# Performance work log

Measured on AMD Instinct MI355X. Metric: run time of the kernel, lower is better.

Reference implementation:

```python
import jax, jax.numpy as jnp
import numpy as np

N_NODES = 50000
N_EDGES = 800000
D_IN = 256
D_H = 128
D_OUT = 2
NUM_FC = 2


def setup_inputs() -> dict:
    key = jax.random.key(0)
    ks = jax.random.split(key, 12)
    s = 0.05
    inp = {
        "x": jax.random.normal(ks[0], (N_NODES, D_IN), dtype=jnp.float32),
        "edge_index": jax.random.randint(ks[1], (2, N_EDGES), 0, N_NODES, dtype=jnp.int64),
        "W_gcn": jax.random.normal(ks[2], (D_IN, D_H), dtype=jnp.float32) * s,
        "b_gcn": jnp.zeros((D_H,), dtype=jnp.float32),
        "fc1_W": jax.random.normal(ks[3], (D_H, D_H), dtype=jnp.float32) * s,
        "fc1_b": jnp.zeros((D_H,), dtype=jnp.float32),
        "fc2_W": jax.random.normal(ks[4], (D_H, D_H), dtype=jnp.float32) * s,
        "fc2_b": jnp.zeros((D_H,), dtype=jnp.float32),
        "out_W": jax.random.normal(ks[5], (D_H, D_OUT), dtype=jnp.float32) * s,
        "out_b": jnp.zeros((D_OUT,), dtype=jnp.float32),
    }
    return inp


def _gcn_conv(x, edge_index, W, b):
    # PyG GCNConv: add self-loops, symmetric normalization D^-1/2 (A+I) D^-1/2, then aggregate X@W.
    n = x.shape[0]
    loops = jnp.arange(n, dtype=edge_index.dtype)
    src = jnp.concatenate([edge_index[0], loops])
    dst = jnp.concatenate([edge_index[1], loops])
    h = x @ W  # [N, D_H]
    deg = jax.ops.segment_sum(jnp.ones_like(dst, dtype=h.dtype), dst, num_segments=n)
    dinv = jnp.where(deg > 0, jax.lax.rsqrt(deg), 0.0)
    norm = dinv[src] * dinv[dst]  # [E+N]
    msg = h[src] * norm[:, None]
    out = jax.ops.segment_sum(msg, dst, num_segments=n)
    return out + b


def _mlp_stack(h, fc1_W, fc1_b, fc2_W, fc2_b):
    # fc -> relu (dropout is eval-mode identity)
    h = jax.nn.relu(h @ fc1_W + fc1_b)
    h = jax.nn.relu(h @ fc2_W + fc2_b)
    return h


def reference(x, edge_index, W_gcn, b_gcn, fc1_W, fc1_b, fc2_W, fc2_b, out_W, out_b):
    h = jax.nn.relu(_gcn_conv(x, edge_index, W_gcn, b_gcn))  # [N, D_H]
    h = _mlp_stack(h, fc1_W, fc1_b, fc2_W, fc2_b)
    # edge-pair gather + average
    edge_x = (h[edge_index[0]] + h[edge_index[1]]) * 0.5  # [E, D_H]
    # note: same fc weights reused, faithful to source
    edge_x = _mlp_stack(edge_x, fc1_W, fc1_b, fc2_W, fc2_b)
    scores = edge_x @ out_W + out_b  # [E, D_OUT]
    return jax.nn.log_softmax(scores, axis=1)
```

## Files before the change

kernel.cpp:

```cpp
#include <hip/hip_runtime.h>

#define NN 50000
#define NE 800000
#define DIN 256
#define DH 128
#define BCAP 64

typedef float f32x4 __attribute__((ext_vector_type(4)));
typedef __bf16 bf16x8 __attribute__((ext_vector_type(8)));
typedef unsigned short u16;
typedef unsigned int u32;

__device__ __forceinline__ u16 f2b(float f) { return __builtin_bit_cast(u16, (__bf16)f); }
__device__ __forceinline__ float lo_f(u32 u) { return (float)__builtin_bit_cast(__bf16, (u16)(u & 0xFFFFu)); }
__device__ __forceinline__ float hi_f(u32 u) { return (float)__builtin_bit_cast(__bf16, (u16)(u >> 16)); }

__device__ __forceinline__ f32x4 mfma16(bf16x8 a, bf16x8 b, f32x4 c) {
    return __builtin_amdgcn_mfma_f32_16x16x32_bf16(a, b, c, 0, 0, 0);
}

__global__ void k_prep_fill(const float* __restrict__ w1, const float* __restrict__ w2,
                            const float* __restrict__ wg,
                            u16* __restrict__ w12f, u16* __restrict__ wgf,
                            const int* __restrict__ ei,
                            int* __restrict__ cnt, int* __restrict__ bucket) {
    int b = blockIdx.x;
    if (b < 32) {
        int t = b * 256 + threadIdx.x;
        const float* src; u16* dst; int id;
        if (t < 2048)      { src = w1; dst = w12f;          id = t; }
        else if (t < 4096) { src = w2; dst = w12f + 16384;  id = t - 2048; }
        else               { src = wg; dst = wgf;           id = t - 4096; }
        int lane = id & 63, frag = id >> 6;
        int kt = frag >> 3, nt = frag & 7;
        int k0 = kt * 32 + (lane >> 4) * 8, n = nt * 16 + (lane & 15);
        u16 v[8];
#pragma unroll
        for (int j = 0; j < 8; ++j) v[j] = f2b(src[(k0 + j) * 128 + n]);
#pragma unroll
        for (int j = 0; j < 8; ++j) dst[id * 8 + j] = v[j];
    } else {
        int e = (b - 32) * 256 + threadIdx.x;
        int d = ei[NE + e];
        int pos = atomicAdd(&cnt[d], 1);
        bucket[d * BCAP + pos] = ei[e];
    }
}

__global__ __launch_bounds__(128) void k_gemm_x(const float* __restrict__ x,
                                                const u16* __restrict__ wgf,
                                                const int* __restrict__ cnt,
                                                u16* __restrict__ h0pre) {
    int wave = threadIdx.x >> 6, lane = threadIdx.x & 63;
    int l15 = lane & 15, q = lane >> 4;
    int rowBase = blockIdx.x * 64 + wave * 32;

    bf16x8 a[2][8];
#pragma unroll
    for (int mi = 0; mi < 2; ++mi) {
        int r = rowBase + mi * 16 + l15; if (r >= NN) r = NN - 1;
        const float* rp = x + (size_t)r * DIN + q * 8;
#pragma unroll
        for (int kt = 0; kt < 8; ++kt) {
            f32x4 f0 = *(const f32x4*)(rp + kt * 32);
            f32x4 f1 = *(const f32x4*)(rp + kt * 32 + 4);
            bf16x8 aa;
#pragma unroll
            for (int j = 0; j < 4; ++j) { aa[j] = (__bf16)f0[j]; aa[j + 4] = (__bf16)f1[j]; }
            a[mi][kt] = aa;
        }
    }
    f32x4 z = {0.f, 0.f, 0.f, 0.f};
    f32x4 acc[2][8];
#pragma unroll
    for (int mi = 0; mi < 2; ++mi)
#pragma unroll
        for (int nt = 0; nt < 8; ++nt) acc[mi][nt] = z;

#pragma unroll
    for (int kt = 0; kt < 8; ++kt)
#pragma unroll
        for (int nt = 0; nt < 8; ++nt) {
            bf16x8 b = *(const bf16x8*)(wgf + ((kt * 8 + nt) * 64 + lane) * 8);
            acc[0][nt] = mfma16(a[0][kt], b, acc[0][nt]);
            acc[1][nt] = mfma16(a[1][kt], b, acc[1][nt]);
        }
#pragma unroll
    for (int mi = 0; mi < 2; ++mi)
#pragma unroll
        for (int rg = 0; rg < 4; ++rg) {
            int r = rowBase + mi * 16 + q * 4 + rg;
            if (r < NN) {
                float dv = rsqrtf((float)cnt[r] + 1.0f);
#pragma unroll
                for (int nt = 0; nt < 8; ++nt)
                    h0pre[r * DH + nt * 16 + l15] = f2b(acc[mi][nt][rg] * dv);
            }
        }
}

__global__ __launch_bounds__(256) void k_aggregate(const u16* __restrict__ h0pre,
                                                   const int* __restrict__ cnt,
                                                   const int* __restrict__ bucket,
                                                   const float* __restrict__ bg,
                                                   u16* __restrict__ hA) {
    int v = blockIdx.x * 4 + (threadIdx.x >> 6);
    int lane = threadIdx.x & 63;
    const u32* h = (const u32*)h0pre;
    u32 su = h[v * 64 + lane];
    float p0[8], p1[8];
#pragma unroll
    for (int k = 0; k < 8; ++k) { p0[k] = 0.f; p1[k] = 0.f; }
    p0[0] = lo_f(su); p1[0] = hi_f(su);
    int deg = cnt[v];
    const int* bk = bucket + v * BCAP;
    int j = 0;
    for (; j + 8 <= deg; j += 8) {
        int idx[8]; u32 u[8];
#pragma unroll
        for (int k = 0; k < 8; ++k) idx[k] = bk[j + k];
#pragma unroll
        for (int k = 0; k < 8; ++k) u[k] = h[idx[k] * 64 + lane];
#pragma unroll
        for (int k = 0; k < 8; ++k) { p0[k] += lo_f(u[k]); p1[k] += hi_f(u[k]); }
    }
    for (; j + 2 <= deg; j += 2) {
        u32 ua = h[bk[j] * 64 + lane];
        u32 ub = h[bk[j + 1] * 64 + lane];
        p0[0] += lo_f(ua); p1[0] += hi_f(ua);
        p0[1] += lo_f(ub); p1[1] += hi_f(ub);
    }
    for (; j < deg; ++j) {
        u32 u = h[bk[j] * 64 + lane];
        p0[0] += lo_f(u); p1[0] += hi_f(u);
    }
#pragma unroll
    for (int k = 4; k >= 1; k >>= 1)
#pragma unroll
        for (int m = 0; m < k; ++m) { p0[m] += p0[m + k]; p1[m] += p1[m + k]; }
    float dv = rsqrtf((float)deg + 1.0f);
    float bg0 = bg[2 * lane], bg1 = bg[2 * lane + 1];
    float a0 = fmaxf(p0[0] * dv + bg0, 0.f);
    float a1 = fmaxf(p1[0] * dv + bg1, 0.f);
    ((u32*)hA)[v * 64 + lane] = (u32)f2b(a0) | ((u32)f2b(a1) << 16);
}

__global__ __launch_bounds__(256) void k_node_mlp(const u16* __restrict__ hA,
                                                  const u16* __restrict__ wf,
                                                  const float* __restrict__ b1,
                                                  const float* __restrict__ b2,
                                                  u16* __restrict__ gh) {
    __shared__ __align__(16) u16 wlds[16384];
    __shared__ __align__(16) u16 sct[4][2176];
    {
        const uint4* s = (const uint4*)wf;
        uint4* d = (uint4*)wlds;
        for (int i = threadIdx.x; i < 2048; i += 256) d[i] = s[i];
    }
    __syncthreads();
    int wave = threadIdx.x >> 6, lane = threadIdx.x & 63;
    int l15 = lane & 15, q = lane >> 4;
    int rowBase = blockIdx.x * 128 + wave * 32;
    u16* sw = sct[wave];

    bf16x8 a[2][4];
#pragma unroll
    for (int mi = 0; mi < 2; ++mi) {
        int r = rowBase + mi * 16 + l15; if (r >= NN) r = NN - 1;
        const u16* rp = hA + r * DH + q * 8;
#pragma unroll
        for (int kt = 0; kt < 4; ++kt) a[mi][kt] = *(const bf16x8*)(rp + kt * 32);
    }
    f32x4 z = {0.f, 0.f, 0.f, 0.f};
    f32x4 acc1[2][8];
#pragma unroll
    for (int mi = 0; mi < 2; ++mi)
#pragma unroll
        for (int nt = 0; nt < 8; ++nt) acc1[mi][nt] = z;
#pragma unroll
    for (int kt = 0; kt < 4; ++kt)
#pragma unroll
        for (int nt = 0; nt < 8; ++nt) {
            bf16x8 b = *(const bf16x8*)(wlds + (kt * 8 + nt) * 512 + lane * 8);
            acc1[0][nt] = mfma16(a[0][kt], b, acc1[0][nt]);
            acc1[1][nt] = mfma16(a[1][kt], b, acc1[1][nt]);
        }
    float bb1[8], bb2[8];
#pragma unroll
    for (int nt = 0; nt < 8; ++nt) { bb1[nt] = b1[nt * 16 + l15]; bb2[nt] = b2[nt * 16 + l15]; }

    bf16x8 a2[2][4];
#pragma unroll
    for (int mi = 0; mi < 2; ++mi) {
#pragma unroll
        for (int nt = 0; nt < 8; ++nt)
#pragma unroll
            for (int rg = 0; rg < 4; ++rg) {
                float v = acc1[mi][nt][rg] + bb1[nt];
                v = v > 0.f ? v : 0.f;
                sw[(q * 4 + rg) * 136 + nt * 16 + l15] = f2b(v);
            }
#pragma unroll
        for (int kt = 0; kt < 4; ++kt)
            a2[mi][kt] = *(const bf16x8*)(sw + l15 * 136 + kt * 32 + q * 8);
    }
    __syncthreads();
    {
        const uint4* s = (const uint4*)(wf + 16384);
        uint4* d = (uint4*)wlds;
        for (int i = threadIdx.x; i < 2048; i += 256) d[i] = s[i];
    }
    __syncthreads();
    f32x4 acc2[2][8];
#pragma unroll
    for (int mi = 0; mi < 2; ++mi)
#pragma unroll
        for (int nt = 0; nt < 8; ++nt) acc2[mi][nt] = z;
#pragma unroll
    for (int kt = 0; kt < 4; ++kt)
#pragma unroll
        for (int nt = 0; nt < 8; ++nt) {
            bf16x8 b = *(const bf16x8*)(wlds + (kt * 8 + nt) * 512 + lane * 8);
            acc2[0][nt] = mfma16(a2[0][kt], b, acc2[0][nt]);
            acc2[1][nt] = mfma16(a2[1][kt], b, acc2[1][nt]);
        }
    bf16x8 a3[2][4];
#pragma unroll
    for (int mi = 0; mi < 2; ++mi) {
#pragma unroll
        for (int nt = 0; nt < 8; ++nt)
#pragma unroll
            for (int rg = 0; rg < 4; ++rg) {
                float v = acc2[mi][nt][rg] + bb2[nt];
                v = v > 0.f ? v : 0.f;
                sw[(q * 4 + rg) * 136 + nt * 16 + l15] = f2b(v);
            }
#pragma unroll
        for (int kt = 0; kt < 4; ++kt)
            a3[mi][kt] = *(const bf16x8*)(sw + l15 * 136 + kt * 32 + q * 8);
    }
    __syncthreads();
    {
        const uint4* s = (const uint4*)wf;
        uint4* d = (uint4*)wlds;
        for (int i = threadIdx.x; i < 2048; i += 256) d[i] = s[i];
    }
    __syncthreads();
    f32x4 acc3[2][8];
#pragma unroll
    for (int mi = 0; mi < 2; ++mi)
#pragma unroll
        for (int nt = 0; nt < 8; ++nt) acc3[mi][nt] = z;
#pragma unroll
    for (int kt = 0; kt < 4; ++kt)
#pragma unroll
        for (int nt = 0; nt < 8; ++nt) {
            bf16x8 b = *(const bf16x8*)(wlds + (kt * 8 + nt) * 512 + lane * 8);
            acc3[0][nt] = mfma16(a3[0][kt], b, acc3[0][nt]);
            acc3[1][nt] = mfma16(a3[1][kt], b, acc3[1][nt]);
        }
#pragma unroll
    for (int mi = 0; mi < 2; ++mi)
#pragma unroll
        for (int nt = 0; nt < 8; ++nt)
#pragma unroll
            for (int rg = 0; rg < 4; ++rg) {
                int r = rowBase + mi * 16 + q * 4 + rg;
                if (r < NN)
                    gh[r * DH + nt * 16 + l15] = f2b(0.5f * acc3[mi][nt][rg] + 0.5f * bb1[nt]);
            }
}

__global__ __launch_bounds__(256, 3) void k_edge_mlp(const u16* __restrict__ gh,
                                                     const int* __restrict__ ei,
                                                     const u16* __restrict__ wf,
                                                     const float* __restrict__ b2,
                                                     const float* __restrict__ ow,
                                                     const float* __restrict__ ob,
                                                     float2* __restrict__ outp) {
    __shared__ __align__(16) u16 wlds[16384];
    {
        const uint4* s = (const uint4*)(wf + 16384);
        uint4* d = (uint4*)wlds;
        for (int i = threadIdx.x; i < 2048; i += 256) d[i] = s[i];
    }
    int wave = threadIdx.x >> 6, lane = threadIdx.x & 63;
    int l15 = lane & 15, q = lane >> 4;
    int eBase = blockIdx.x * 256 + wave * 64;

    int se[4], de[4];
#pragma unroll
    for (int ti = 0; ti < 4; ++ti) {
        int e = eBase + ti * 16 + l15;
        se[ti] = ei[e];
        de[ti] = ei[NE + e];
    }
    bf16x8 gsA[4], gdA[4], gsB[4], gdB[4];
    {
        const u16* ps = gh + se[0] * DH + q * 8;
        const u16* pd = gh + de[0] * DH + q * 8;
#pragma unroll
        for (int kt = 0; kt < 4; ++kt) {
            gsA[kt] = *(const bf16x8*)(ps + kt * 32);
            gdA[kt] = *(const bf16x8*)(pd + kt * 32);
        }
    }
    {
        const u16* ps = gh + se[1] * DH + q * 8;
        const u16* pd = gh + de[1] * DH + q * 8;
#pragma unroll
        for (int kt = 0; kt < 4; ++kt) {
            gsB[kt] = *(const bf16x8*)(ps + kt * 32);
            gdB[kt] = *(const bf16x8*)(pd + kt * 32);
        }
    }
    float bb2[8], owp0[8], owp1[8];
#pragma unroll
    for (int nt = 0; nt < 8; ++nt) {
        int k = nt * 16 + l15;
        bb2[nt] = b2[k];
        owp0[nt] = ow[2 * k];
        owp1[nt] = ow[2 * k + 1];
    }
    float ob0 = ob[0], ob1 = ob[1];
    __syncthreads();
    f32x4 z = {0.f, 0.f, 0.f, 0.f};

#pragma unroll
    for (int ti = 0; ti < 4; ++ti) {
        bf16x8 fs[4], fd[4];
#pragma unroll
        for (int kt = 0; kt < 4; ++kt) {
            fs[kt] = (ti & 1) ? gsB[kt] : gsA[kt];
            fd[kt] = (ti & 1) ? gdB[kt] : gdA[kt];
        }
        if (ti + 2 < 4) {
            const u16* ps = gh + se[ti + 2] * DH + q * 8;
            const u16* pd = gh + de[ti + 2] * DH + q * 8;
#pragma unroll
            for (int kt = 0; kt < 4; ++kt) {
                if (ti & 1) { gsB[kt] = *(const bf16x8*)(ps + kt * 32); gdB[kt] = *(const bf16x8*)(pd + kt * 32); }
                else        { gsA[kt] = *(const bf16x8*)(ps + kt * 32); gdA[kt] = *(const bf16x8*)(pd + kt * 32); }
            }
        }
        bf16x8 a2[4];
#pragma unroll
        for (int kt = 0; kt < 4; ++kt) {
            bf16x8 r;
#pragma unroll
            for (int j = 0; j < 8; ++j) {
                float t = (float)fs[kt][j] + (float)fd[kt][j];
                r[j] = (__bf16)(t > 0.f ? t : 0.f);
            }
            a2[kt] = r;
        }
        f32x4 acc2[8];
#pragma unroll
        for (int nt = 0; nt < 8; ++nt) acc2[nt] = z;
#pragma unroll
        for (int kt = 0; kt < 4; ++kt)
#pragma unroll
            for (int nt = 0; nt < 8; ++nt) {
                bf16x8 b = *(const bf16x8*)(wlds + (kt * 8 + nt) * 512 + lane * 8);
                acc2[nt] = mfma16(a2[kt], b, acc2[nt]);
            }
#pragma unroll
        for (int rg = 0; rg < 4; ++rg) {
            float p0 = 0.f, p1 = 0.f;
#pragma unroll
            for (int nt = 0; nt < 8; ++nt) {
                float t = acc2[nt][rg] + bb2[nt];
                t = t > 0.f ? t : 0.f;
                p0 += t * owp0[nt];
                p1 += t * owp1[nt];
            }
#pragma unroll
            for (int m = 1; m < 16; m <<= 1) {
                p0 += __shfl_xor(p0, m, 64);
                p1 += __shfl_xor(p1, m, 64);
            }
            if (l15 == 0) {
                int e = eBase + ti * 16 + q * 4 + rg;
                float s0 = p0 + ob0, s1 = p1 + ob1;
                float mx = fmaxf(s0, s1);
                float lse = mx + __logf(__expf(s0 - mx) + __expf(s1 - mx));
                outp[e] = make_float2(s0 - lse, s1 - lse);
            }
        }
    }
}

extern "C" void kernel_launch(void* const* d_in, const int* in_sizes, int n_in,
                              void* d_out, int out_size, void* d_ws, size_t ws_size,
                              hipStream_t stream) {
    const float* x  = (const float*)d_in[0];
    const int* ei   = (const int*)d_in[1];
    const float* wg = (const float*)d_in[2];
    const float* bg = (const float*)d_in[3];
    const float* w1 = (const float*)d_in[4];
    const float* b1 = (const float*)d_in[5];
    const float* w2 = (const float*)d_in[6];
    const float* b2 = (const float*)d_in[7];
    const float* ow = (const float*)d_in[8];
    const float* ob = (const float*)d_in[9];
    float2* out = (float2*)d_out;

    char* ws = (char*)d_ws;
    size_t off = 0;
    auto alloc = [&](size_t bytes) { void* p = ws + off; off += (bytes + 255) & ~(size_t)255; return p; };
    u16* h0      = (u16*)alloc((size_t)NN * DH * 2);
    u16* hA      = (u16*)alloc((size_t)NN * DH * 2);
    int* bucket  = (int*)alloc((size_t)NN * BCAP * 4);
    int* cnt     = (int*)alloc((size_t)NN * 4);
    u16* w12f    = (u16*)alloc(65536);
    u16* wgf     = (u16*)alloc(65536);
    u16* gh      = h0;

    hipMemsetAsync(cnt, 0, (size_t)NN * 4, stream);
    k_prep_fill<<<32 + NE / 256, 256, 0, stream>>>(w1, w2, wg, w12f, wgf, ei, cnt, bucket);
    k_gemm_x<<<(NN + 63) / 64, 128, 0, stream>>>(x, wgf, cnt, h0);
    k_aggregate<<<NN / 4, 256, 0, stream>>>(h0, cnt, bucket, bg, hA);
    k_node_mlp<<<(NN + 127) / 128, 256, 0, stream>>>(hA, w12f, b1, b2, gh);
    k_edge_mlp<<<NE / 256, 256, 0, stream>>>(gh, ei, w12f, b2, ow, ob, out);
}
```

Measured before the change: 305.1 us.

## Process edges grouped by destination bucket in edge MLP for gather locality

The edge MLP kernel now walks edges through the destination-sorted buckets (storing source and edge id pairs) instead of original edge order. Each wave handles eight destination nodes, so destination rows are reused and hit in cache. In exchange, the bucket array doubles in size, each edge needs an index lookup, the scores are written scattered by edge id, and per-wave work varies with node degree, leaving partially filled tiles.

```diff
diff --git a/kernel.cpp b/kernel.cpp
--- a/kernel.cpp
+++ b/kernel.cpp
@@ -23,7 +23,7 @@
                             const float* __restrict__ wg,
                             u16* __restrict__ w12f, u16* __restrict__ wgf,
                             const int* __restrict__ ei,
-                            int* __restrict__ cnt, int* __restrict__ bucket) {
+                            int* __restrict__ cnt, int2* __restrict__ bucket) {
     int b = blockIdx.x;
     if (b < 32) {
         int t = b * 256 + threadIdx.x;
@@ -42,8 +42,9 @@
     } else {
         int e = (b - 32) * 256 + threadIdx.x;
         int d = ei[NE + e];
+        int s = ei[e];
         int pos = atomicAdd(&cnt[d], 1);
-        bucket[d * BCAP + pos] = ei[e];
+        bucket[d * BCAP + pos] = make_int2(s, e);
     }
 }
 
@@ -101,7 +102,7 @@
 
 __global__ __launch_bounds__(256) void k_aggregate(const u16* __restrict__ h0pre,
                                                    const int* __restrict__ cnt,
-                                                   const int* __restrict__ bucket,
+                                                   const int2* __restrict__ bucket,
                                                    const float* __restrict__ bg,
                                                    u16* __restrict__ hA) {
     int v = blockIdx.x * 4 + (threadIdx.x >> 6);
@@ -113,25 +114,25 @@
     for (int k = 0; k < 8; ++k) { p0[k] = 0.f; p1[k] = 0.f; }
     p0[0] = lo_f(su); p1[0] = hi_f(su);
     int deg = cnt[v];
-    const int* bk = bucket + v * BCAP;
+    const int2* bk = bucket + v * BCAP;
     int j = 0;
     for (; j + 8 <= deg; j += 8) {
         int idx[8]; u32 u[8];
 #pragma unroll
-        for (int k = 0; k < 8; ++k) idx[k] = bk[j + k];
+        for (int k = 0; k < 8; ++k) idx[k] = bk[j + k].x;
 #pragma unroll
         for (int k = 0; k < 8; ++k) u[k] = h[idx[k] * 64 + lane];
 #pragma unroll
         for (int k = 0; k < 8; ++k) { p0[k] += lo_f(u[k]); p1[k] += hi_f(u[k]); }
     }
     for (; j + 2 <= deg; j += 2) {
-        u32 ua = h[bk[j] * 64 + lane];
-        u32 ub = h[bk[j + 1] * 64 + lane];
+        u32 ua = h[bk[j].x * 64 + lane];
+        u32 ub = h[bk[j + 1].x * 64 + lane];
         p0[0] += lo_f(ua); p1[0] += hi_f(ua);
         p0[1] += lo_f(ub); p1[1] += hi_f(ub);
     }
     for (; j < deg; ++j) {
-        u32 u = h[bk[j] * 64 + lane];
+        u32 u = h[bk[j].x * 64 + lane];
         p0[0] += lo_f(u); p1[0] += hi_f(u);
     }
 #pragma unroll
@@ -272,7 +273,8 @@
 }
 
 __global__ __launch_bounds__(256, 3) void k_edge_mlp(const u16* __restrict__ gh,
-                                                     const int* __restrict__ ei,
+                                                     const int2* __restrict__ bucket,
+                                                     const int* __restrict__ cnt,
                                                      const u16* __restrict__ wf,
                                                      const float* __restrict__ b2,
                                                      const float* __restrict__ ow,
@@ -286,28 +288,42 @@
     }
     int wave = threadIdx.x >> 6, lane = threadIdx.x & 63;
     int l15 = lane & 15, q = lane >> 4;
-    int eBase = blockIdx.x * 256 + wave * 64;
-
-    int se[4], de[4];
-#pragma unroll
-    for (int ti = 0; ti < 4; ++ti) {
-        int e = eBase + ti * 16 + l15;
-        se[ti] = ei[e];
-        de[ti] = ei[NE + e];
-    }
+    int dstBase = blockIdx.x * 32 + wave * 8;
+
+    int c = 0;
+    if (lane < 8) { int d = dstBase + lane; c = (d < NN) ? cnt[d] : 0; }
+    int s[9]; s[0] = 0;
+#pragma unroll
+    for (int i = 0; i < 8; ++i) { int ci = __shfl(c, i, 64); s[i + 1] = s[i] + ci; }
+    int T = s[8];
+    int nT = (T + 15) >> 4;
+
+    auto fetch = [&](int t, int& src, int& dst, int& e) {
+        if (t < T) {
+            int d = 0;
+#pragma unroll
+            for (int i = 1; i < 8; ++i) d += (t >= s[i]);
+            int2 be = bucket[(dstBase + d) * BCAP + (t - s[d])];
+            src = be.x; e = be.y; dst = dstBase + d;
+        } else { src = 0; dst = 0; e = -1; }
+    };
+
+    int srcA, dstA, eA, srcB, dstB, eB;
     bf16x8 gsA[4], gdA[4], gsB[4], gdB[4];
-    {
-        const u16* ps = gh + se[0] * DH + q * 8;
-        const u16* pd = gh + de[0] * DH + q * 8;
+    fetch(l15, srcA, dstA, eA);
+    {
+        const u16* ps = gh + srcA * DH + q * 8;
+        const u16* pd = gh + dstA * DH + q * 8;
 #pragma unroll
         for (int kt = 0; kt < 4; ++kt) {
             gsA[kt] = *(const bf16x8*)(ps + kt * 32);
             gdA[kt] = *(const bf16x8*)(pd + kt * 32);
         }
     }
-    {
-        const u16* ps = gh + se[1] * DH + q * 8;
-        const u16* pd = gh + de[1] * DH + q * 8;
+    fetch(16 + l15, srcB, dstB, eB);
+    {
+        const u16* ps = gh + srcB * DH + q * 8;
+        const u16* pd = gh + dstB * DH + q * 8;
 #pragma unroll
         for (int kt = 0; kt < 4; ++kt) {
             gsB[kt] = *(const bf16x8*)(ps + kt * 32);
@@ -326,21 +342,31 @@
     __syncthreads();
     f32x4 z = {0.f, 0.f, 0.f, 0.f};
 
-#pragma unroll
-    for (int ti = 0; ti < 4; ++ti) {
+    for (int t = 0; t < nT; ++t) {
         bf16x8 fs[4], fd[4];
-#pragma unroll
-        for (int kt = 0; kt < 4; ++kt) {
-            fs[kt] = (ti & 1) ? gsB[kt] : gsA[kt];
-            fd[kt] = (ti & 1) ? gdB[kt] : gdA[kt];
-        }
-        if (ti + 2 < 4) {
-            const u16* ps = gh + se[ti + 2] * DH + q * 8;
-            const u16* pd = gh + de[ti + 2] * DH + q * 8;
-#pragma unroll
-            for (int kt = 0; kt < 4; ++kt) {
-                if (ti & 1) { gsB[kt] = *(const bf16x8*)(ps + kt * 32); gdB[kt] = *(const bf16x8*)(pd + kt * 32); }
-                else        { gsA[kt] = *(const bf16x8*)(ps + kt * 32); gdA[kt] = *(const bf16x8*)(pd + kt * 32); }
+        int eCur;
+        if (t & 1) {
+#pragma unroll
+            for (int kt = 0; kt < 4; ++kt) { fs[kt] = gsB[kt]; fd[kt] = gdB[kt]; }
+            eCur = eB;
+        } else {
+#pragma unroll
+            for (int kt = 0; kt < 4; ++kt) { fs[kt] = gsA[kt]; fd[kt] = gdA[kt]; }
+            eCur = eA;
+        }
+        if (t + 2 < nT) {
+            int srcN, dstN, eN;
+            fetch((t + 2) * 16 + l15, srcN, dstN, eN);
+            const u16* ps = gh + srcN * DH + q * 8;
+            const u16* pd = gh + dstN * DH + q * 8;
+            if (t & 1) {
+#pragma unroll
+                for (int kt = 0; kt < 4; ++kt) { gsB[kt] = *(const bf16x8*)(ps + kt * 32); gdB[kt] = *(const bf16x8*)(pd + kt * 32); }
+                eB = eN;
+            } else {
+#pragma unroll
+                for (int kt = 0; kt < 4; ++kt) { gsA[kt] = *(const bf16x8*)(ps + kt * 32); gdA[kt] = *(const bf16x8*)(pd + kt * 32); }
+                eA = eN;
             }
         }
         bf16x8 a2[4];
@@ -349,8 +375,8 @@
             bf16x8 r;
 #pragma unroll
             for (int j = 0; j < 8; ++j) {
-                float t = (float)fs[kt][j] + (float)fd[kt][j];
-                r[j] = (__bf16)(t > 0.f ? t : 0.f);
+                float tt = (float)fs[kt][j] + (float)fd[kt][j];
+                r[j] = (__bf16)(tt > 0.f ? tt : 0.f);
             }
             a2[kt] = r;
         }
@@ -369,22 +395,21 @@
             float p0 = 0.f, p1 = 0.f;
 #pragma unroll
             for (int nt = 0; nt < 8; ++nt) {
-                float t = acc2[nt][rg] + bb2[nt];
-                t = t > 0.f ? t : 0.f;
-                p0 += t * owp0[nt];
-                p1 += t * owp1[nt];
+                float tt = acc2[nt][rg] + bb2[nt];
+                tt = tt > 0.f ? tt : 0.f;
+                p0 += tt * owp0[nt];
+                p1 += tt * owp1[nt];
             }
 #pragma unroll
             for (int m = 1; m < 16; m <<= 1) {
                 p0 += __shfl_xor(p0, m, 64);
                 p1 += __shfl_xor(p1, m, 64);
             }
-            if (l15 == 0) {
-                int e = eBase + ti * 16 + q * 4 + rg;
+            if (l15 == q * 4 + rg && eCur >= 0) {
                 float s0 = p0 + ob0, s1 = p1 + ob1;
                 float mx = fmaxf(s0, s1);
                 float lse = mx + __logf(__expf(s0 - mx) + __expf(s1 - mx));
-                outp[e] = make_float2(s0 - lse, s1 - lse);
+                outp[eCur] = make_float2(s0 - lse, s1 - lse);
             }
         }
     }
@@ -410,7 +435,7 @@
     auto alloc = [&](size_t bytes) { void* p = ws + off; off += (bytes + 255) & ~(size_t)255; return p; };
     u16* h0      = (u16*)alloc((size_t)NN * DH * 2);
     u16* hA      = (u16*)alloc((size_t)NN * DH * 2);
-    int* bucket  = (int*)alloc((size_t)NN * BCAP * 4);
+    int2* bucket = (int2*)alloc((size_t)NN * BCAP * 8);
     int* cnt     = (int*)alloc((size_t)NN * 4);
     u16* w12f    = (u16*)alloc(65536);
     u16* wgf     = (u16*)alloc(65536);
@@ -421,5 +446,5 @@
     k_gemm_x<<<(NN + 63) / 64, 128, 0, stream>>>(x, wgf, cnt, h0);
     k_aggregate<<<NN / 4, 256, 0, stream>>>(h0, cnt, bucket, bg, hA);
     k_node_mlp<<<(NN + 127) / 128, 256, 0, stream>>>(hA, w12f, b1, b2, gh);
-    k_edge_mlp<<<NE / 256, 256, 0, stream>>>(gh, ei, w12f, b2, ow, ob, out);
-}
+    k_edge_mlp<<<(NN + 31) / 32, 256, 0, stream>>>(gh, bucket, cnt, w12f, b2, ow, ob, out);
+}
```

Result: slower. 610.7 us (+100.2%).
